# Kernel tuning notes

Hardware: AMD Instinct MI355X
Metric: run time of the kernel (lower is better)

Reference implementation:

```python
import jax, jax.numpy as jnp
import numpy as np
import math

WS = 8          # window size
DIM = 32        # per-head dim
NH = 8          # num_head
TH = 16         # total_head
B, H, W = 4, 128, 128
WA = WS * WS    # window area


def _rel_pos_index():
    coords = np.stack(np.meshgrid(np.arange(WS), np.arange(WS), indexing='ij'))  # (2, WS, WS)
    cf = coords.reshape(2, -1)                      # (2, WA)
    rc = cf[:, :, None] - cf[:, None, :]            # (2, WA, WA)
    rc = rc.transpose(1, 2, 0).copy()               # (WA, WA, 2)
    rc[:, :, 0] += WS - 1
    rc[:, :, 1] += WS - 1
    rc[:, :, 0] *= 2 * WS - 1
    return rc.sum(-1)                               # (WA, WA)


def setup_inputs() -> dict:
    key = jax.random.key(0)
    k1, k2, k3, k4 = jax.random.split(key, 4)
    qkv = jax.random.normal(k1, (B, NH, 3 * DIM, H, W), dtype=jnp.float32)
    ch = jax.random.normal(k2, (B, (TH - NH) * DIM, H, W), dtype=jnp.float32)
    logit_scale = jnp.log(10.0) * jnp.ones((NH, 1, 1), dtype=jnp.float32)
    rel_bias_table = 0.02 * jax.random.normal(k3, ((2 * WS - 1) ** 2, NH), dtype=jnp.float32)
    proj_w = 0.02 * jax.random.normal(k4, (NH * DIM, NH * DIM), dtype=jnp.float32)  # 1x1 conv
    proj_b = jnp.zeros((NH * DIM,), dtype=jnp.float32)
    rel_index = jnp.asarray(_rel_pos_index(), dtype=jnp.int32)
    return {"qkv": qkv, "ch": ch, "logit_scale": logit_scale,
            "rel_bias_table": rel_bias_table, "proj_w": proj_w,
            "proj_b": proj_b, "rel_index": rel_index}


def _window_partition(x):
    # x: (B, l, c, H, W) -> (B*nh*nw, l, WA, c)
    b, l, c, h, w = x.shape
    nh, nw = h // WS, w // WS
    x = x.reshape(b, l, c, nh, WS, nw, WS)
    x = x.transpose(0, 3, 5, 1, 4, 6, 2)            # b, nh, nw, l, wh, ww, c
    return x.reshape(b * nh * nw, l, WA, c)


def _l2norm(x):
    n = jnp.sqrt(jnp.sum(x * x, axis=-1, keepdims=True))
    return x / jnp.maximum(n, 1e-12)


def reference(qkv, ch, logit_scale, rel_bias_table, proj_w, proj_b, rel_index):
    b, L, C3, h, w = qkv.shape
    nh, nw = h // WS, w // WS
    qkvw = _window_partition(qkv)                   # (Bw, L, WA, 3*DIM)
    q, k, v = jnp.split(qkvw, 3, axis=-1)           # each (Bw, L, WA, DIM)

    # helper gating
    lch = TH - NH
    chw = _window_partition(ch.reshape(b, lch, DIM, h, w))  # (Bw, lch, WA, DIM)
    chm = jnp.mean(chw, axis=1, keepdims=True)      # (Bw, 1, WA, DIM)
    v = v * chm

    # cosine attention
    attn = jnp.einsum('wlqc,wlkc->wlqk', _l2norm(q), _l2norm(k))
    scale = jnp.exp(jnp.minimum(logit_scale, math.log(1.0 / 0.01)))  # (L,1,1)
    bias = rel_bias_table[rel_index.reshape(-1)].reshape(WA, WA, NH)
    bias = bias.transpose(2, 0, 1)[None]            # (1, L, WA, WA)
    attn = jax.nn.softmax(attn * scale[None] + bias, axis=-1)
    x = jnp.einsum('wlqk,wlkc->wlqc', attn, v)      # (Bw, L, WA, DIM)

    # window unpartition -> (B, L*DIM, H, W)
    x = x.reshape(b, nh, nw, L, WS, WS, DIM)
    x = x.transpose(0, 3, 6, 1, 4, 2, 5)            # b, l, c, nh, wh, nw, ww
    x = x.reshape(b, L * DIM, h, w)

    # 1x1 conv projection
    x = jnp.einsum('bchw,oc->bohw', x, proj_w) + proj_b[None, :, None, None]
    return x
```

## Files before the change

### kernel.cpp

```cpp
#include <hip/hip_runtime.h>


typedef __attribute__((ext_vector_type(8))) short short8v;
typedef __attribute__((ext_vector_type(4))) float f32x4;
typedef __attribute__((ext_vector_type(2))) unsigned int u32x2;

#define PLANE 16384
#define LOG100 4.6051701859880914f

static __device__ __forceinline__ unsigned short f2bf(float x) {
  union { float f; unsigned u; } v; v.f = x;
  unsigned r = v.u + 0x7fff + ((v.u >> 16) & 1);
  return (unsigned short)(r >> 16);
}
static __device__ __forceinline__ float bf2f(unsigned short b) {
  union { unsigned u; float f; } v; v.u = ((unsigned)b) << 16;
  return v.f;
}

__global__ __launch_bounds__(256) void prep_kernel(
    const float* __restrict__ ch, const float* __restrict__ btab,
    const int* __restrict__ ridx, const float* __restrict__ pw,
    float* __restrict__ chm, float* __restrict__ biasG,
    unsigned int* __restrict__ wbf)
{
  const int blk = blockIdx.x, tid = threadIdx.x;
  if (blk < 2048) {
    int idx = blk * 256 + tid;
    int b = idx >> 17, c = (idx >> 12) & 31, p4 = idx & 4095;
    const float4* s0 = (const float4*)ch + ((size_t)(b * 256 + c)) * (PLANE / 4) + p4;
    float4 a = {0.f, 0.f, 0.f, 0.f};
#pragma unroll
    for (int l = 0; l < 8; ++l) {
      float4 t = s0[(size_t)(l * 32) * (PLANE / 4)];
      a.x += t.x; a.y += t.y; a.z += t.z; a.w += t.w;
    }
    a.x *= 0.125f; a.y *= 0.125f; a.z *= 0.125f; a.w *= 0.125f;
    ((float4*)chm)[((size_t)(b * 32 + c)) * (PLANE / 4) + p4] = a;
  } else if (blk < 2176) {
    int i = (blk - 2048) * 256 + tid;
    int h = i >> 12, qk = i & 4095;
    biasG[i] = btab[ridx[qk] * 8 + h];
  } else {
    int i = (blk - 2176) * 256 + tid;
    wbf[i] = (unsigned)f2bf(pw[2 * i]) | ((unsigned)f2bf(pw[2 * i + 1]) << 16);
  }
}

__global__ __launch_bounds__(512) void fused_kernel(
    const float* __restrict__ qkv, const float* __restrict__ chm,
    const float* __restrict__ lsc, const float* __restrict__ biasG,
    const unsigned short* __restrict__ wbf, const float* __restrict__ pb,
    float* __restrict__ out)
{
  __shared__ __align__(16) char smem[32768];

  const int tid = threadIdx.x;
  const int orig = blockIdx.x;
  const int win = ((orig & 7) << 7) | (orig >> 3);
  const int b  = win >> 8;
  const int wy = (win >> 4) & 15;
  const int wx = win & 15;
  const int y0 = wy << 3, x0 = wx << 3;

  const int h = tid >> 6, lane = tid & 63;
  const int lg = lane >> 4, lr = lane & 15;

  const size_t qbase = ((size_t)((b * 8 + h) * 96)) * PLANE;
  const float* qg = qkv + qbase;
  const float* kg = qg + (size_t)32 * PLANE;
  const float* vg = qg + (size_t)64 * PLANE;
  const float* cg = chm + (size_t)(b * 32) * PLANE;
  const float scale = __expf(fminf(lsc[h], LOG100));

  short8v vf[2][2];
#pragma unroll
  for (int dt = 0; dt < 2; ++dt) {
    const int d = 16 * dt + lr;
    const float* vp = vg + (size_t)d * PLANE;
    const float* cp = cg + (size_t)d * PLANE;
#pragma unroll
    for (int m = 0; m < 2; ++m) {
      int ka = 4 * lg + 32 * m, kb = ka + 16;
      int spa = (y0 + (ka >> 3)) * 128 + x0 + (ka & 7);
      int spb = (y0 + (kb >> 3)) * 128 + x0 + (kb & 7);
      float4 va = *(const float4*)(vp + spa);
      float4 ca = *(const float4*)(cp + spa);
      float4 vb = *(const float4*)(vp + spb);
      float4 cb = *(const float4*)(cp + spb);
      vf[dt][m][0] = (short)f2bf(va.x * ca.x);
      vf[dt][m][1] = (short)f2bf(va.y * ca.y);
      vf[dt][m][2] = (short)f2bf(va.z * ca.z);
      vf[dt][m][3] = (short)f2bf(va.w * ca.w);
      vf[dt][m][4] = (short)f2bf(vb.x * cb.x);
      vf[dt][m][5] = (short)f2bf(vb.y * cb.y);
      vf[dt][m][6] = (short)f2bf(vb.z * cb.z);
      vf[dt][m][7] = (short)f2bf(vb.w * cb.w);
    }
  }

  float qq[4][8];
#pragma unroll
  for (int st = 0; st < 4; ++st) {
    int q = 16 * st + lr;
    int spq = (y0 + (q >> 3)) * 128 + x0 + (q & 7);
#pragma unroll
    for (int j = 0; j < 8; ++j)
      qq[st][j] = qg[(size_t)(8 * lg + j) * PLANE + spq];
  }
  float kk[4][8];
#pragma unroll
  for (int kt = 0; kt < 4; ++kt) {
    int kpos = 16 * kt + lr;
    int spk = (y0 + (kpos >> 3)) * 128 + x0 + (kpos & 7);
#pragma unroll
    for (int j = 0; j < 8; ++j)
      kk[kt][j] = kg[(size_t)(8 * lg + j) * PLANE + spk];
  }

  short8v khi[4], klo[4];
#pragma unroll
  for (int kt = 0; kt < 4; ++kt) {
    float nr = 0.f;
#pragma unroll
    for (int j = 0; j < 8; ++j) nr = fmaf(kk[kt][j], kk[kt][j], nr);
    nr += __shfl_xor(nr, 16);
    nr += __shfl_xor(nr, 32);
    float iv = 1.f / fmaxf(sqrtf(nr), 1e-12f);
#pragma unroll
    for (int j = 0; j < 8; ++j) {
      float x = kk[kt][j] * iv;
      unsigned short hb = f2bf(x);
      khi[kt][j] = (short)hb;
      klo[kt][j] = (short)f2bf(x - bf2f(hb));
    }
  }

  const float* bgh = biasG + (h << 12);

#pragma unroll 1
  for (int st = 0; st < 4; ++st) {
    const int q = 16 * st + lr;

    float nrq = 0.f;
#pragma unroll
    for (int j = 0; j < 8; ++j) nrq = fmaf(qq[st][j], qq[st][j], nrq);
    nrq += __shfl_xor(nrq, 16);
    nrq += __shfl_xor(nrq, 32);
    const float fq = scale / fmaxf(sqrtf(nrq), 1e-12f);

    short8v qhi, qlo;
#pragma unroll
    for (int j = 0; j < 8; ++j) {
      float x = qq[st][j] * fq;
      unsigned short hb = f2bf(x);
      qhi[j] = (short)hb;
      qlo[j] = (short)f2bf(x - bf2f(hb));
    }

    const float4* bq = (const float4*)(bgh + (q << 6));
    float e[16], mx = -1e30f;
#pragma unroll
    for (int kt = 0; kt < 4; ++kt) {
      f32x4 a = {0.f, 0.f, 0.f, 0.f};
      a = __builtin_amdgcn_mfma_f32_16x16x32_bf16(klo[kt], qhi, a, 0, 0, 0);
      a = __builtin_amdgcn_mfma_f32_16x16x32_bf16(khi[kt], qlo, a, 0, 0, 0);
      a = __builtin_amdgcn_mfma_f32_16x16x32_bf16(khi[kt], qhi, a, 0, 0, 0);
      float4 b4 = bq[4 * kt + lg];
      float bb[4] = {b4.x, b4.y, b4.z, b4.w};
#pragma unroll
      for (int r = 0; r < 4; ++r) {
        float lv = a[r] + bb[r];
        e[4 * kt + r] = lv;
        mx = fmaxf(mx, lv);
      }
    }
    mx = fmaxf(mx, __shfl_xor(mx, 16));
    mx = fmaxf(mx, __shfl_xor(mx, 32));
    float s = 0.f;
#pragma unroll
    for (int i = 0; i < 16; ++i) { e[i] = __expf(e[i] - mx); s += e[i]; }
    s += __shfl_xor(s, 16);
    s += __shfl_xor(s, 32);
    float rl = 1.f / s;

    short8v pf[2];
#pragma unroll
    for (int m = 0; m < 2; ++m)
#pragma unroll
      for (int j = 0; j < 8; ++j)
        pf[m][j] = (short)f2bf(e[4 * (j >> 2) + 8 * m + (j & 3)]);

    const int pl = q;
#pragma unroll
    for (int dt = 0; dt < 2; ++dt) {
      f32x4 o = {0.f, 0.f, 0.f, 0.f};
      o = __builtin_amdgcn_mfma_f32_16x16x32_bf16(vf[dt][0], pf[0], o, 0, 0, 0);
      o = __builtin_amdgcn_mfma_f32_16x16x32_bf16(vf[dt][1], pf[1], o, 0, 0, 0);
      u32x2 ww;
      ww[0] = (unsigned)f2bf(o[0] * rl) | ((unsigned)f2bf(o[1] * rl) << 16);
      ww[1] = (unsigned)f2bf(o[2] * rl) | ((unsigned)f2bf(o[3] * rl) << 16);
      unsigned off = (unsigned)(pl * 512)
                   + (((unsigned)(64 * h + 32 * dt + 8 * lg)) ^ ((unsigned)(pl & 7) << 4));
      *(u32x2*)(smem + off) = ww;
    }
  }
  __syncthreads();

  f32x4 acc[2][4];
#pragma unroll
  for (int i = 0; i < 2; ++i)
#pragma unroll
    for (int j = 0; j < 4; ++j) acc[i][j] = (f32x4){0.f, 0.f, 0.f, 0.f};

#pragma unroll 1
  for (int kc = 0; kc < 8; ++kc) {
    short8v wf0 = *(const short8v*)(wbf + (size_t)(32 * h + lr) * 256 + 32 * kc + 8 * lg);
    short8v wf1 = *(const short8v*)(wbf + (size_t)(32 * h + 16 + lr) * 256 + 32 * kc + 8 * lg);
    short8v xf[4];
#pragma unroll
    for (int pt = 0; pt < 4; ++pt) {
      int pl = 16 * pt + lr;
      unsigned off = (unsigned)(pl * 512)
                   + (((unsigned)(64 * kc + 16 * lg)) ^ ((unsigned)(pl & 7) << 4));
      xf[pt] = *(const short8v*)(smem + off);
    }
#pragma unroll
    for (int pt = 0; pt < 4; ++pt) {
      acc[0][pt] = __builtin_amdgcn_mfma_f32_16x16x32_bf16(wf0, xf[pt], acc[0][pt], 0, 0, 0);
      acc[1][pt] = __builtin_amdgcn_mfma_f32_16x16x32_bf16(wf1, xf[pt], acc[1][pt], 0, 0, 0);
    }
  }

#pragma unroll
  for (int ot = 0; ot < 2; ++ot) {
#pragma unroll
    for (int r = 0; r < 4; ++r) {
      int o = 32 * h + 16 * ot + 4 * lg + r;
      float bv = pb[o];
      float* op = out + ((size_t)(b * 256 + o)) * PLANE;
#pragma unroll
      for (int pt = 0; pt < 4; ++pt) {
        int p = 16 * pt + lr;
        op[(y0 + (p >> 3)) * 128 + x0 + (p & 7)] = acc[ot][pt][r] + bv;
      }
    }
  }
}

extern "C" void kernel_launch(void* const* d_in, const int* in_sizes, int n_in,
                              void* d_out, int out_size, void* d_ws, size_t ws_size,
                              hipStream_t stream) {
  const float* qkv  = (const float*)d_in[0];
  const float* ch   = (const float*)d_in[1];
  const float* lsc  = (const float*)d_in[2];
  const float* btab = (const float*)d_in[3];
  const float* pw   = (const float*)d_in[4];
  const float* pb   = (const float*)d_in[5];
  const int*   ridx = (const int*)d_in[6];
  float* out = (float*)d_out;

  char* ws = (char*)d_ws;
  float*          biasG = (float*)ws;
  unsigned short* wbf   = (unsigned short*)(ws + 131072);
  float*          chm   = (float*)(ws + 262144);

  prep_kernel<<<dim3(2304), dim3(256), 0, stream>>>(ch, btab, ridx, pw,
                                                    chm, biasG, (unsigned int*)wbf);
  fused_kernel<<<dim3(1024), dim3(512), 0, stream>>>(qkv, chm, lsc, biasG,
                                                     wbf, pb, out);
}
```

Baseline: 133.8 us.

## Halve block to 4 waves, each processing two heads with prefetched Q

Blocks drop from 512 to 256 threads, so each wave handles two heads in sequence and computes 64 output channels in the projection instead of 32. Q rows are software-prefetched one step ahead, and the manual bf16 rounding is replaced with packed hardware conversion intrinsics. s_setprio hints are placed around the MFMA sections. The intent is higher occupancy (launch bounds of 4 blocks) and less conversion ALU work, in exchange for more serial work per wave.

```diff
diff --git a/kernel.cpp b/kernel.cpp
--- a/kernel.cpp
+++ b/kernel.cpp
@@ -1,21 +1,30 @@
 #include <hip/hip_runtime.h>
+#include <hip/hip_bf16.h>
 
 
 typedef __attribute__((ext_vector_type(8))) short short8v;
 typedef __attribute__((ext_vector_type(4))) float f32x4;
+typedef __attribute__((ext_vector_type(4))) unsigned int u32x4;
 typedef __attribute__((ext_vector_type(2))) unsigned int u32x2;
 
 #define PLANE 16384
 #define LOG100 4.6051701859880914f
 
-static __device__ __forceinline__ unsigned short f2bf(float x) {
-  union { float f; unsigned u; } v; v.f = x;
-  unsigned r = v.u + 0x7fff + ((v.u >> 16) & 1);
-  return (unsigned short)(r >> 16);
-}
-static __device__ __forceinline__ float bf2f(unsigned short b) {
-  union { unsigned u; float f; } v; v.u = ((unsigned)b) << 16;
-  return v.f;
+static __device__ __forceinline__ unsigned pk2(float a, float b) {
+  float2 t; t.x = a; t.y = b;
+  __hip_bfloat162 r = __float22bfloat162_rn(t);
+  unsigned u;
+  __builtin_memcpy(&u, &r, 4);
+  return u;
+}
+struct HiLo { unsigned hi, lo; };
+static __device__ __forceinline__ HiLo split2(float x0, float x1) {
+  HiLo o;
+  o.hi = pk2(x0, x1);
+  float h0 = __builtin_bit_cast(float, o.hi << 16);
+  float h1 = __builtin_bit_cast(float, o.hi & 0xffff0000u);
+  o.lo = pk2(x0 - h0, x1 - h1);
+  return o;
 }
 
 __global__ __launch_bounds__(256) void prep_kernel(
@@ -43,11 +52,11 @@
     biasG[i] = btab[ridx[qk] * 8 + h];
   } else {
     int i = (blk - 2176) * 256 + tid;
-    wbf[i] = (unsigned)f2bf(pw[2 * i]) | ((unsigned)f2bf(pw[2 * i + 1]) << 16);
+    wbf[i] = pk2(pw[2 * i], pw[2 * i + 1]);
   }
 }
 
-__global__ __launch_bounds__(512) void fused_kernel(
+__global__ __launch_bounds__(256, 4) void fused_kernel(
     const float* __restrict__ qkv, const float* __restrict__ chm,
     const float* __restrict__ lsc, const float* __restrict__ biasG,
     const unsigned short* __restrict__ wbf, const float* __restrict__ pb,
@@ -63,160 +72,182 @@
   const int wx = win & 15;
   const int y0 = wy << 3, x0 = wx << 3;
 
-  const int h = tid >> 6, lane = tid & 63;
+  const int wv = tid >> 6, lane = tid & 63;
   const int lg = lane >> 4, lr = lane & 15;
 
-  const size_t qbase = ((size_t)((b * 8 + h) * 96)) * PLANE;
-  const float* qg = qkv + qbase;
-  const float* kg = qg + (size_t)32 * PLANE;
-  const float* vg = qg + (size_t)64 * PLANE;
   const float* cg = chm + (size_t)(b * 32) * PLANE;
-  const float scale = __expf(fminf(lsc[h], LOG100));
-
-  short8v vf[2][2];
-#pragma unroll
-  for (int dt = 0; dt < 2; ++dt) {
-    const int d = 16 * dt + lr;
-    const float* vp = vg + (size_t)d * PLANE;
-    const float* cp = cg + (size_t)d * PLANE;
-#pragma unroll
-    for (int m = 0; m < 2; ++m) {
-      int ka = 4 * lg + 32 * m, kb = ka + 16;
-      int spa = (y0 + (ka >> 3)) * 128 + x0 + (ka & 7);
-      int spb = (y0 + (kb >> 3)) * 128 + x0 + (kb & 7);
-      float4 va = *(const float4*)(vp + spa);
-      float4 ca = *(const float4*)(cp + spa);
-      float4 vb = *(const float4*)(vp + spb);
-      float4 cb = *(const float4*)(cp + spb);
-      vf[dt][m][0] = (short)f2bf(va.x * ca.x);
-      vf[dt][m][1] = (short)f2bf(va.y * ca.y);
-      vf[dt][m][2] = (short)f2bf(va.z * ca.z);
-      vf[dt][m][3] = (short)f2bf(va.w * ca.w);
-      vf[dt][m][4] = (short)f2bf(vb.x * cb.x);
-      vf[dt][m][5] = (short)f2bf(vb.y * cb.y);
-      vf[dt][m][6] = (short)f2bf(vb.z * cb.z);
-      vf[dt][m][7] = (short)f2bf(vb.w * cb.w);
-    }
-  }
-
-  float qq[4][8];
-#pragma unroll
-  for (int st = 0; st < 4; ++st) {
-    int q = 16 * st + lr;
-    int spq = (y0 + (q >> 3)) * 128 + x0 + (q & 7);
-#pragma unroll
-    for (int j = 0; j < 8; ++j)
-      qq[st][j] = qg[(size_t)(8 * lg + j) * PLANE + spq];
-  }
-  float kk[4][8];
-#pragma unroll
-  for (int kt = 0; kt < 4; ++kt) {
-    int kpos = 16 * kt + lr;
-    int spk = (y0 + (kpos >> 3)) * 128 + x0 + (kpos & 7);
-#pragma unroll
-    for (int j = 0; j < 8; ++j)
-      kk[kt][j] = kg[(size_t)(8 * lg + j) * PLANE + spk];
-  }
-
-  short8v khi[4], klo[4];
-#pragma unroll
-  for (int kt = 0; kt < 4; ++kt) {
-    float nr = 0.f;
-#pragma unroll
-    for (int j = 0; j < 8; ++j) nr = fmaf(kk[kt][j], kk[kt][j], nr);
-    nr += __shfl_xor(nr, 16);
-    nr += __shfl_xor(nr, 32);
-    float iv = 1.f / fmaxf(sqrtf(nr), 1e-12f);
-#pragma unroll
-    for (int j = 0; j < 8; ++j) {
-      float x = kk[kt][j] * iv;
-      unsigned short hb = f2bf(x);
-      khi[kt][j] = (short)hb;
-      klo[kt][j] = (short)f2bf(x - bf2f(hb));
-    }
-  }
-
-  const float* bgh = biasG + (h << 12);
 
 #pragma unroll 1
-  for (int st = 0; st < 4; ++st) {
-    const int q = 16 * st + lr;
-
-    float nrq = 0.f;
-#pragma unroll
-    for (int j = 0; j < 8; ++j) nrq = fmaf(qq[st][j], qq[st][j], nrq);
-    nrq += __shfl_xor(nrq, 16);
-    nrq += __shfl_xor(nrq, 32);
-    const float fq = scale / fmaxf(sqrtf(nrq), 1e-12f);
-
-    short8v qhi, qlo;
-#pragma unroll
-    for (int j = 0; j < 8; ++j) {
-      float x = qq[st][j] * fq;
-      unsigned short hb = f2bf(x);
-      qhi[j] = (short)hb;
-      qlo[j] = (short)f2bf(x - bf2f(hb));
-    }
-
-    const float4* bq = (const float4*)(bgh + (q << 6));
-    float e[16], mx = -1e30f;
+  for (int hh = 0; hh < 2; ++hh) {
+    const int h = wv + 4 * hh;
+    const size_t qbase = ((size_t)((b * 8 + h) * 96)) * PLANE;
+    const float* qg = qkv + qbase;
+    const float* kg = qg + (size_t)32 * PLANE;
+    const float* vg = qg + (size_t)64 * PLANE;
+    const float scale = __expf(fminf(lsc[h], LOG100));
+
+    short8v vf[2][2];
+#pragma unroll
+    for (int dt = 0; dt < 2; ++dt) {
+      const int d = 16 * dt + lr;
+      const float* vp = vg + (size_t)d * PLANE;
+      const float* cp = cg + (size_t)d * PLANE;
+#pragma unroll
+      for (int m = 0; m < 2; ++m) {
+        int ka = 4 * lg + 32 * m, kb = ka + 16;
+        int spa = (y0 + (ka >> 3)) * 128 + x0 + (ka & 7);
+        int spb = (y0 + (kb >> 3)) * 128 + x0 + (kb & 7);
+        float4 va = *(const float4*)(vp + spa);
+        float4 ca = *(const float4*)(cp + spa);
+        float4 vb = *(const float4*)(vp + spb);
+        float4 cb = *(const float4*)(cp + spb);
+        u32x4 u;
+        u[0] = pk2(va.x * ca.x, va.y * ca.y);
+        u[1] = pk2(va.z * ca.z, va.w * ca.w);
+        u[2] = pk2(vb.x * cb.x, vb.y * cb.y);
+        u[3] = pk2(vb.z * cb.z, vb.w * cb.w);
+        vf[dt][m] = __builtin_bit_cast(short8v, u);
+      }
+    }
+
+    short8v khi[4], klo[4];
 #pragma unroll
     for (int kt = 0; kt < 4; ++kt) {
-      f32x4 a = {0.f, 0.f, 0.f, 0.f};
-      a = __builtin_amdgcn_mfma_f32_16x16x32_bf16(klo[kt], qhi, a, 0, 0, 0);
-      a = __builtin_amdgcn_mfma_f32_16x16x32_bf16(khi[kt], qlo, a, 0, 0, 0);
-      a = __builtin_amdgcn_mfma_f32_16x16x32_bf16(khi[kt], qhi, a, 0, 0, 0);
-      float4 b4 = bq[4 * kt + lg];
-      float bb[4] = {b4.x, b4.y, b4.z, b4.w};
-#pragma unroll
-      for (int r = 0; r < 4; ++r) {
-        float lv = a[r] + bb[r];
-        e[4 * kt + r] = lv;
-        mx = fmaxf(mx, lv);
-      }
-    }
-    mx = fmaxf(mx, __shfl_xor(mx, 16));
-    mx = fmaxf(mx, __shfl_xor(mx, 32));
-    float s = 0.f;
-#pragma unroll
-    for (int i = 0; i < 16; ++i) { e[i] = __expf(e[i] - mx); s += e[i]; }
-    s += __shfl_xor(s, 16);
-    s += __shfl_xor(s, 32);
-    float rl = 1.f / s;
-
-    short8v pf[2];
-#pragma unroll
-    for (int m = 0; m < 2; ++m)
+      int kpos = 16 * kt + lr;
+      int spk = (y0 + (kpos >> 3)) * 128 + x0 + (kpos & 7);
+      float kk[8];
 #pragma unroll
       for (int j = 0; j < 8; ++j)
-        pf[m][j] = (short)f2bf(e[4 * (j >> 2) + 8 * m + (j & 3)]);
-
-    const int pl = q;
-#pragma unroll
-    for (int dt = 0; dt < 2; ++dt) {
-      f32x4 o = {0.f, 0.f, 0.f, 0.f};
-      o = __builtin_amdgcn_mfma_f32_16x16x32_bf16(vf[dt][0], pf[0], o, 0, 0, 0);
-      o = __builtin_amdgcn_mfma_f32_16x16x32_bf16(vf[dt][1], pf[1], o, 0, 0, 0);
-      u32x2 ww;
-      ww[0] = (unsigned)f2bf(o[0] * rl) | ((unsigned)f2bf(o[1] * rl) << 16);
-      ww[1] = (unsigned)f2bf(o[2] * rl) | ((unsigned)f2bf(o[3] * rl) << 16);
-      unsigned off = (unsigned)(pl * 512)
-                   + (((unsigned)(64 * h + 32 * dt + 8 * lg)) ^ ((unsigned)(pl & 7) << 4));
-      *(u32x2*)(smem + off) = ww;
+        kk[j] = kg[(size_t)(8 * lg + j) * PLANE + spk];
+      float nr = 0.f;
+#pragma unroll
+      for (int j = 0; j < 8; ++j) nr = fmaf(kk[j], kk[j], nr);
+      nr += __shfl_xor(nr, 16);
+      nr += __shfl_xor(nr, 32);
+      float iv = 1.f / fmaxf(sqrtf(nr), 1e-12f);
+      u32x4 uh, ul;
+#pragma unroll
+      for (int p2 = 0; p2 < 4; ++p2) {
+        HiLo hl = split2(kk[2 * p2] * iv, kk[2 * p2 + 1] * iv);
+        uh[p2] = hl.hi;
+        ul[p2] = hl.lo;
+      }
+      khi[kt] = __builtin_bit_cast(short8v, uh);
+      klo[kt] = __builtin_bit_cast(short8v, ul);
+    }
+
+    const float* bgh = biasG + (h << 12);
+
+    float qa[8], qb[8];
+    {
+      int spq = (y0 + (lr >> 3)) * 128 + x0 + (lr & 7);
+#pragma unroll
+      for (int j = 0; j < 8; ++j)
+        qa[j] = qg[(size_t)(8 * lg + j) * PLANE + spq];
+    }
+#pragma unroll 1
+    for (int st = 0; st < 4; ++st) {
+      if (st < 3) {
+        int qn = 16 * (st + 1) + lr;
+        int spq = (y0 + (qn >> 3)) * 128 + x0 + (qn & 7);
+#pragma unroll
+        for (int j = 0; j < 8; ++j)
+          qb[j] = qg[(size_t)(8 * lg + j) * PLANE + spq];
+      }
+      const int q = 16 * st + lr;
+
+      float nrq = 0.f;
+#pragma unroll
+      for (int j = 0; j < 8; ++j) nrq = fmaf(qa[j], qa[j], nrq);
+      nrq += __shfl_xor(nrq, 16);
+      nrq += __shfl_xor(nrq, 32);
+      const float fq = scale / fmaxf(sqrtf(nrq), 1e-12f);
+
+      short8v qhi, qlo;
+      {
+        u32x4 uh, ul;
+#pragma unroll
+        for (int p2 = 0; p2 < 4; ++p2) {
+          HiLo hl = split2(qa[2 * p2] * fq, qa[2 * p2 + 1] * fq);
+          uh[p2] = hl.hi;
+          ul[p2] = hl.lo;
+        }
+        qhi = __builtin_bit_cast(short8v, uh);
+        qlo = __builtin_bit_cast(short8v, ul);
+      }
+
+      const float4* bq = (const float4*)(bgh + (q << 6));
+      float e[16], mx = -1e30f;
+      __builtin_amdgcn_s_setprio(1);
+#pragma unroll
+      for (int kt = 0; kt < 4; ++kt) {
+        f32x4 a = {0.f, 0.f, 0.f, 0.f};
+        a = __builtin_amdgcn_mfma_f32_16x16x32_bf16(klo[kt], qhi, a, 0, 0, 0);
+        a = __builtin_amdgcn_mfma_f32_16x16x32_bf16(khi[kt], qlo, a, 0, 0, 0);
+        a = __builtin_amdgcn_mfma_f32_16x16x32_bf16(khi[kt], qhi, a, 0, 0, 0);
+        float4 b4 = bq[4 * kt + lg];
+        float bb[4] = {b4.x, b4.y, b4.z, b4.w};
+#pragma unroll
+        for (int r = 0; r < 4; ++r) {
+          float lv = a[r] + bb[r];
+          e[4 * kt + r] = lv;
+          mx = fmaxf(mx, lv);
+        }
+      }
+      __builtin_amdgcn_s_setprio(0);
+      mx = fmaxf(mx, __shfl_xor(mx, 16));
+      mx = fmaxf(mx, __shfl_xor(mx, 32));
+      float s = 0.f;
+#pragma unroll
+      for (int i = 0; i < 16; ++i) { e[i] = __expf(e[i] - mx); s += e[i]; }
+      s += __shfl_xor(s, 16);
+      s += __shfl_xor(s, 32);
+      float rl = 1.f / s;
+
+      short8v pf[2];
+#pragma unroll
+      for (int m = 0; m < 2; ++m) {
+        u32x4 up;
+#pragma unroll
+        for (int p2 = 0; p2 < 4; ++p2)
+          up[p2] = pk2(e[8 * m + 2 * p2], e[8 * m + 2 * p2 + 1]);
+        pf[m] = __builtin_bit_cast(short8v, up);
+      }
+
+      const int pl = q;
+      __builtin_amdgcn_s_setprio(1);
+#pragma unroll
+      for (int dt = 0; dt < 2; ++dt) {
+        f32x4 o = {0.f, 0.f, 0.f, 0.f};
+        o = __builtin_amdgcn_mfma_f32_16x16x32_bf16(vf[dt][0], pf[0], o, 0, 0, 0);
+        o = __builtin_amdgcn_mfma_f32_16x16x32_bf16(vf[dt][1], pf[1], o, 0, 0, 0);
+        u32x2 ww;
+        ww[0] = pk2(o[0] * rl, o[1] * rl);
+        ww[1] = pk2(o[2] * rl, o[3] * rl);
+        unsigned off = (unsigned)(pl * 512)
+                     + (((unsigned)(64 * h + 32 * dt + 8 * lg)) ^ ((unsigned)(pl & 7) << 4));
+        *(u32x2*)(smem + off) = ww;
+      }
+      __builtin_amdgcn_s_setprio(0);
+
+#pragma unroll
+      for (int j = 0; j < 8; ++j) qa[j] = qb[j];
     }
   }
   __syncthreads();
 
-  f32x4 acc[2][4];
-#pragma unroll
-  for (int i = 0; i < 2; ++i)
+  f32x4 acc[4][4];
+#pragma unroll
+  for (int i = 0; i < 4; ++i)
 #pragma unroll
     for (int j = 0; j < 4; ++j) acc[i][j] = (f32x4){0.f, 0.f, 0.f, 0.f};
 
 #pragma unroll 1
   for (int kc = 0; kc < 8; ++kc) {
-    short8v wf0 = *(const short8v*)(wbf + (size_t)(32 * h + lr) * 256 + 32 * kc + 8 * lg);
-    short8v wf1 = *(const short8v*)(wbf + (size_t)(32 * h + 16 + lr) * 256 + 32 * kc + 8 * lg);
+    short8v wf[4];
+#pragma unroll
+    for (int ot = 0; ot < 4; ++ot)
+      wf[ot] = *(const short8v*)(wbf + (size_t)(64 * wv + 16 * ot + lr) * 256 + 32 * kc + 8 * lg);
     short8v xf[4];
 #pragma unroll
     for (int pt = 0; pt < 4; ++pt) {
@@ -225,18 +256,20 @@
                    + (((unsigned)(64 * kc + 16 * lg)) ^ ((unsigned)(pl & 7) << 4));
       xf[pt] = *(const short8v*)(smem + off);
     }
-#pragma unroll
-    for (int pt = 0; pt < 4; ++pt) {
-      acc[0][pt] = __builtin_amdgcn_mfma_f32_16x16x32_bf16(wf0, xf[pt], acc[0][pt], 0, 0, 0);
-      acc[1][pt] = __builtin_amdgcn_mfma_f32_16x16x32_bf16(wf1, xf[pt], acc[1][pt], 0, 0, 0);
-    }
+    __builtin_amdgcn_s_setprio(1);
+#pragma unroll
+    for (int ot = 0; ot < 4; ++ot)
+#pragma unroll
+      for (int pt = 0; pt < 4; ++pt)
+        acc[ot][pt] = __builtin_amdgcn_mfma_f32_16x16x32_bf16(wf[ot], xf[pt], acc[ot][pt], 0, 0, 0);
+    __builtin_amdgcn_s_setprio(0);
   }
 
 #pragma unroll
-  for (int ot = 0; ot < 2; ++ot) {
+  for (int ot = 0; ot < 4; ++ot) {
 #pragma unroll
     for (int r = 0; r < 4; ++r) {
-      int o = 32 * h + 16 * ot + 4 * lg + r;
+      int o = 64 * wv + 16 * ot + 4 * lg + r;
       float bv = pb[o];
       float* op = out + ((size_t)(b * 256 + o)) * PLANE;
 #pragma unroll
@@ -267,6 +300,6 @@
 
   prep_kernel<<<dim3(2304), dim3(256), 0, stream>>>(ch, btab, ridx, pw,
                                                     chm, biasG, (unsigned int*)wbf);
-  fused_kernel<<<dim3(1024), dim3(512), 0, stream>>>(qkv, chm, lsc, biasG,
+  fused_kernel<<<dim3(1024), dim3(256), 0, stream>>>(qkv, chm, lsc, biasG,
                                                      wbf, pb, out);
 }
```

After: 145.1 us. 1.08x slower.
